# Performance work log

Measured on AMD Instinct MI355X. Metric: run time of the kernel, lower is better.

Reference implementation:

```python
import jax, jax.numpy as jnp
import numpy as np
import math

B, S, D, H = 8, 2048, 256, 8

def setup_inputs() -> dict:
    key = jax.random.key(0)
    k1, k2, k3 = jax.random.split(key, 3)
    e = jax.random.normal(k1, (B, S, D), dtype=jnp.float32)
    p = jax.random.normal(k2, (B, S + 1, D), dtype=jnp.float32)
    n_layer = 12
    W_o = jax.random.normal(k3, (D, D * H), dtype=jnp.float32) * (0.02 / math.sqrt(2 * n_layer))
    return {"e": e, "p": p, "W_o": W_o}

def reference(e, p, W_o):
    # e: [B,S,D], p: [B,S+1,D], W_o: [D, H*D] (nn.Linear weight)
    Bx, Sx, Dx = e.shape
    Hh = W_o.shape[1] // Dx
    # Original builds head-replicated Q=p, K=p[:-1], V=e; all heads compute
    # identical attention, so compute it once and tile for the W_o mix.
    q = p[:, 1:, :]   # rows 1..S of Q survive the [:, :, 1:, :] slice
    k = p[:, :-1, :]  # [B,S,D]
    scores = jnp.einsum('bqd,bkd->bqk', q, k) / math.sqrt(Dx)  # [B,S,S]
    scores = jnp.clip(scores, -10.0, 10.0)  # clamp happens BEFORE masking
    # Mask: tril(diag=-1) rows 1..S-1 plus an all-ones last row == standard
    # causal mask (col <= row) after the row slice.
    causal = jnp.tril(jnp.ones((Sx, Sx), dtype=bool))
    scores = jnp.where(causal[None, :, :], scores, -jnp.inf)
    attn = jax.nn.softmax(scores, axis=-1)
    y = jnp.einsum('bqk,bkd->bqd', attn, e)  # [B,S,D]
    # W_N diagonal matmul == per-row scale by 1/(i+1)
    row_scale = 1.0 / (jnp.arange(Sx, dtype=y.dtype) + 1.0)
    y = y * row_scale[None, :, None]
    y_cat = jnp.tile(y, (1, 1, Hh))  # heads are identical -> [B,S,H*D]
    out = y_cat @ W_o.T  # Linear(H*D -> D), no bias
    return out
```

## Files before the change

### kernel.cpp

```cpp
#include <hip/hip_runtime.h>


typedef __attribute__((ext_vector_type(8))) short short8;
typedef __attribute__((ext_vector_type(4))) float f32x4;

__device__ __forceinline__ unsigned short f2b(float x) {
  unsigned u = __builtin_bit_cast(unsigned, x);
  u = (u + 0x7fffu + ((u >> 16) & 1u)) >> 16;
  return (unsigned short)u;
}

__global__ void cvt_p_kernel(const float* __restrict__ src, unsigned short* __restrict__ dst) {
  size_t t = (size_t)blockIdx.x * 256 + threadIdx.x;
  const float4* s = (const float4*)(src + t * 8);
  float4 a = s[0], b = s[1];
  short8 o;
  o[0] = (short)f2b(a.x); o[1] = (short)f2b(a.y); o[2] = (short)f2b(a.z); o[3] = (short)f2b(a.w);
  o[4] = (short)f2b(b.x); o[5] = (short)f2b(b.y); o[6] = (short)f2b(b.z); o[7] = (short)f2b(b.w);
  *(short8*)(dst + t * 8) = o;
}

__global__ void perm_e_kernel(const float* __restrict__ e, unsigned short* __restrict__ dst) {
  size_t t = (size_t)blockIdx.x * 256 + threadIdx.x;
  int lane = (int)(t & 63);
  int d0 = (int)((t >> 6) & 15);
  int kt = (int)((t >> 10) & 63);
  int b = (int)(t >> 16);
  int g = lane >> 4, l = lane & 15;
  const float* s = e + ((size_t)b * 2048 + kt * 32 + g * 8) * 256 + d0 * 16 + l;
  short8 o;
#pragma unroll
  for (int i = 0; i < 8; ++i) o[i] = (short)f2b(s[(size_t)i * 256]);
  *(short8*)(dst + t * 8) = o;
}

__global__ void perm_k_kernel(const float* __restrict__ p, unsigned short* __restrict__ dst) {
  size_t t = (size_t)blockIdx.x * 256 + threadIdx.x;
  int lane = (int)(t & 63);
  int idx = (int)((t >> 6) & 15);
  int kt = (int)((t >> 10) & 63);
  int b = (int)(t >> 16);
  int kc = idx >> 1, n0 = idx & 1;
  int g = lane >> 4, l = lane & 15;
  const float* s = p + ((size_t)b * 2049 + kt * 32 + n0 * 16 + l) * 256 + kc * 32 + g * 8;
  float4 a = *(const float4*)s;
  float4 c = *(const float4*)(s + 4);
  short8 o;
  o[0] = (short)f2b(a.x); o[1] = (short)f2b(a.y); o[2] = (short)f2b(a.z); o[3] = (short)f2b(a.w);
  o[4] = (short)f2b(c.x); o[5] = (short)f2b(c.y); o[6] = (short)f2b(c.z); o[7] = (short)f2b(c.w);
  *(short8*)(dst + t * 8) = o;
}

__global__ void fold_w_kernel(const float* __restrict__ w, unsigned short* __restrict__ dst) {
  int d = blockIdx.x;
  int c = threadIdx.x;
  const float* row = w + (size_t)d * 2048 + c;
  float s = 0.f;
#pragma unroll
  for (int h = 0; h < 8; ++h) s += row[h * 256];
  dst[d * 256 + c] = f2b(s);
}

#define SMEM_BYTES 25088

__global__ __launch_bounds__(256, 2) void attn_main_kernel(const unsigned short* __restrict__ pbf,
                                                           const unsigned short* __restrict__ kperm,
                                                           const unsigned short* __restrict__ eperm,
                                                           const unsigned short* __restrict__ wsum,
                                                           float* __restrict__ out) {
  __shared__ char smem[SMEM_BYTES];
  const int b = blockIdx.x & 7;
  const int j0 = blockIdx.x >> 3;
  const int t16 = (j0 < 64) ? j0 : 191 - j0;
  const int qbase = t16 * 16;
  const int nkt = (t16 >> 1) + 1;
  const int wave = threadIdx.x >> 6;
  const int lane = threadIdx.x & 63;
  const int g = lane >> 4;
  const int l = lane & 15;
  const f32x4 zero = {0.f, 0.f, 0.f, 0.f};

  short8 qf[8];
  {
    const unsigned short* qrow = pbf + ((size_t)b * 2049 + qbase + l + 1) * 256;
#pragma unroll
    for (int kc = 0; kc < 8; ++kc) qf[kc] = *(const short8*)(qrow + kc * 32 + g * 8);
  }

  f32x4 yacc[16];
#pragma unroll
  for (int i = 0; i < 16; ++i) yacc[i] = zero;
  float dsum[4] = {0.f, 0.f, 0.f, 0.f};

  unsigned short* pp = (unsigned short*)(smem + 16384 + wave * 1280);
  const unsigned short* kpool = kperm + (size_t)b * 64 * 8192 + (size_t)lane * 8;
  const unsigned short* epool = eperm + (size_t)b * 64 * 8192 + (size_t)lane * 8;

  short8 kf[16], ef[16];
  if (wave < nkt) {
    const unsigned short* kb = kpool + (size_t)wave * 8192;
    const unsigned short* eb = epool + (size_t)wave * 8192;
#pragma unroll
    for (int i = 0; i < 16; ++i) kf[i] = *(const short8*)(kb + i * 512);
#pragma unroll
    for (int i = 0; i < 16; ++i) ef[i] = *(const short8*)(eb + i * 512);
  }

  for (int kt = wave; kt < nkt; kt += 4) {
    const int ktn = kt + 4;
    f32x4 sacc0 = zero, sacc1 = zero;
#pragma unroll
    for (int kc = 0; kc < 8; ++kc) {
      sacc0 = __builtin_amdgcn_mfma_f32_16x16x32_bf16(qf[kc], kf[kc * 2 + 0], sacc0, 0, 0, 0);
      sacc1 = __builtin_amdgcn_mfma_f32_16x16x32_bf16(qf[kc], kf[kc * 2 + 1], sacc1, 0, 0, 0);
    }
    if (ktn < nkt) {
      const unsigned short* kb = kpool + (size_t)ktn * 8192;
#pragma unroll
      for (int i = 0; i < 16; ++i) kf[i] = *(const short8*)(kb + i * 512);
    }
#pragma unroll
    for (int n0 = 0; n0 < 2; ++n0) {
      const int kg = kt * 32 + n0 * 16 + l;
      const f32x4 sv = n0 ? sacc1 : sacc0;
#pragma unroll
      for (int jj = 0; jj < 4; ++jj) {
        float s = sv[jj] * 0.0625f;
        s = fminf(fmaxf(s, -10.f), 10.f);
        const int qg = qbase + g * 4 + jj;
        float w = (kg <= qg) ? __expf(s) : 0.f;
        dsum[jj] += w;
        pp[(g * 4 + jj) * 40 + n0 * 16 + l] = f2b(w);
      }
    }
    short8 af = *(const short8*)((const unsigned short*)pp + l * 40 + g * 8);
#pragma unroll
    for (int d0 = 0; d0 < 16; ++d0)
      yacc[d0] = __builtin_amdgcn_mfma_f32_16x16x32_bf16(af, ef[d0], yacc[d0], 0, 0, 0);
    if (ktn < nkt) {
      const unsigned short* eb = epool + (size_t)ktn * 8192;
#pragma unroll
      for (int i = 0; i < 16; ++i) ef[i] = *(const short8*)(eb + i * 512);
    }
  }

#pragma unroll
  for (int jj = 0; jj < 4; ++jj) {
    float v = dsum[jj];
    v += __shfl_xor(v, 1);
    v += __shfl_xor(v, 2);
    v += __shfl_xor(v, 4);
    v += __shfl_xor(v, 8);
    dsum[jj] = v;
  }
  float* dbuf = (float*)(smem + 24832);
  if (wave != 0 && l == 0) {
#pragma unroll
    for (int jj = 0; jj < 4; ++jj) dbuf[(wave - 1) * 16 + g * 4 + jj] = dsum[jj];
  }

  f32x4* bufv = (f32x4*)smem;
  __syncthreads();
  if (wave == 1) {
#pragma unroll
    for (int d0 = 0; d0 < 16; ++d0) bufv[d0 * 64 + lane] = yacc[d0];
  }
  __syncthreads();
  if (wave == 0) {
#pragma unroll
    for (int d0 = 0; d0 < 16; ++d0) yacc[d0] += bufv[d0 * 64 + lane];
  }
  __syncthreads();
  if (wave == 2) {
#pragma unroll
    for (int d0 = 0; d0 < 16; ++d0) bufv[d0 * 64 + lane] = yacc[d0];
  }
  __syncthreads();
  if (wave == 0) {
#pragma unroll
    for (int d0 = 0; d0 < 16; ++d0) yacc[d0] += bufv[d0 * 64 + lane];
  }
  __syncthreads();
  if (wave == 3) {
#pragma unroll
    for (int d0 = 0; d0 < 16; ++d0) bufv[d0 * 64 + lane] = yacc[d0];
  }
  __syncthreads();
  unsigned short* py = (unsigned short*)(smem + 16384);
  if (wave == 0) {
    float inv[4];
#pragma unroll
    for (int jj = 0; jj < 4; ++jj) {
      float dtot = dsum[jj] + dbuf[g * 4 + jj] + dbuf[16 + g * 4 + jj] + dbuf[32 + g * 4 + jj];
      const int qg = qbase + g * 4 + jj;
      inv[jj] = 1.f / (dtot * (float)(qg + 1));
    }
#pragma unroll
    for (int d0 = 0; d0 < 16; ++d0) {
      f32x4 yt = yacc[d0] + bufv[d0 * 64 + lane];
#pragma unroll
      for (int jj = 0; jj < 4; ++jj)
        py[(g * 4 + jj) * 264 + d0 * 16 + l] = f2b(yt[jj] * inv[jj]);
    }
  }
  __syncthreads();

  {
    f32x4 oacc[4];
#pragma unroll
    for (int i = 0; i < 4; ++i) oacc[i] = zero;
#pragma unroll
    for (int kc = 0; kc < 8; ++kc) {
      short8 a2 = *(const short8*)(py + l * 264 + kc * 32 + g * 8);
#pragma unroll
      for (int dd = 0; dd < 4; ++dd) {
        short8 wf =
            *(const short8*)(wsum + (size_t)((wave * 4 + dd) * 16 + l) * 256 + kc * 32 + g * 8);
        oacc[dd] = __builtin_amdgcn_mfma_f32_16x16x32_bf16(a2, wf, oacc[dd], 0, 0, 0);
      }
    }
#pragma unroll
    for (int dd = 0; dd < 4; ++dd) {
#pragma unroll
      for (int jj = 0; jj < 4; ++jj) {
        const int qg = qbase + g * 4 + jj;
        const int d = (wave * 4 + dd) * 16 + l;
        out[((size_t)b * 2048 + qg) * 256 + d] = oacc[dd][jj];
      }
    }
  }
}

extern "C" void kernel_launch(void* const* d_in, const int* in_sizes, int n_in, void* d_out,
                              int out_size, void* d_ws, size_t ws_size, hipStream_t stream) {
  (void)in_sizes; (void)n_in; (void)out_size; (void)ws_size;
  const float* e = (const float*)d_in[0];
  const float* p = (const float*)d_in[1];
  const float* Wo = (const float*)d_in[2];
  float* out = (float*)d_out;

  unsigned short* pbf = (unsigned short*)d_ws;
  unsigned short* eperm = (unsigned short*)((char*)d_ws + 8392704);
  unsigned short* kperm = (unsigned short*)((char*)d_ws + 16781312);
  unsigned short* wsum = (unsigned short*)((char*)d_ws + 25169920);

  hipLaunchKernelGGL(cvt_p_kernel, dim3(2049), dim3(256), 0, stream, p, pbf);
  hipLaunchKernelGGL(perm_e_kernel, dim3(2048), dim3(256), 0, stream, e, eperm);
  hipLaunchKernelGGL(perm_k_kernel, dim3(2048), dim3(256), 0, stream, p, kperm);
  hipLaunchKernelGGL(fold_w_kernel, dim3(256), dim3(256), 0, stream, Wo, wsum);
  hipLaunchKernelGGL(attn_main_kernel, dim3(1024), dim3(256), 0, stream, pbf, kperm, eperm, wsum,
                     out);
}
```

Before: 149.6 us.

## Stage K/V tiles in LDS with double buffering, 32-row query blocks

The attention kernel now gives each block 32 query rows, split across two query-halves of two waves each. K and V tiles are streamed into double-buffered shared memory with global_load_lds, replacing per-wave register prefetch of whole tiles. Each wave covers one 16-column half of the scores and half of the output dimensions, so waves share the staged tiles and the four-way cross-wave reduction of the y accumulators goes away. The cost is more shared memory (about 67KB per block), which may cap occupancy, a barrier every K tile, and half as many blocks in the grid.

```diff
diff --git a/kernel.cpp b/kernel.cpp
--- a/kernel.cpp
+++ b/kernel.cpp
@@ -9,6 +9,10 @@
   u = (u + 0x7fffu + ((u >> 16) & 1u)) >> 16;
   return (unsigned short)u;
 }
+
+#define GLOAD_LDS16(gp, lp)                                                                        \
+  __builtin_amdgcn_global_load_lds((const __attribute__((address_space(1))) unsigned int*)(gp),    \
+                                   (__attribute__((address_space(3))) unsigned int*)(lp), 16, 0, 0)
 
 __global__ void cvt_p_kernel(const float* __restrict__ src, unsigned short* __restrict__ dst) {
   size_t t = (size_t)blockIdx.x * 256 + threadIdx.x;
@@ -61,7 +65,22 @@
   dst[d * 256 + c] = f2b(s);
 }
 
-#define SMEM_BYTES 25088
+#define SMEM_BYTES 68352
+
+__device__ __forceinline__ void stage_tile(char* smem, int s, int b, int kt, int tid,
+                                           const unsigned short* kperm,
+                                           const unsigned short* eperm) {
+  const size_t cb = (size_t)(b * 64 + kt) * 8192;
+  char* kd = smem + s * 32768;
+  const char* ks = (const char*)(kperm + cb);
+  const char* es = (const char*)(eperm + cb);
+  const int wv64 = tid & ~63;
+#pragma unroll
+  for (int j = 0; j < 4; ++j) {
+    GLOAD_LDS16(ks + (j * 256 + tid) * 16, kd + (j * 256 + wv64) * 16);
+    GLOAD_LDS16(es + (j * 256 + tid) * 16, kd + 16384 + (j * 256 + wv64) * 16);
+  }
+}
 
 __global__ __launch_bounds__(256, 2) void attn_main_kernel(const unsigned short* __restrict__ pbf,
                                                            const unsigned short* __restrict__ kperm,
@@ -70,78 +89,71 @@
                                                            float* __restrict__ out) {
   __shared__ char smem[SMEM_BYTES];
   const int b = blockIdx.x & 7;
-  const int j0 = blockIdx.x >> 3;
-  const int t16 = (j0 < 64) ? j0 : 191 - j0;
-  const int qbase = t16 * 16;
-  const int nkt = (t16 >> 1) + 1;
-  const int wave = threadIdx.x >> 6;
-  const int lane = threadIdx.x & 63;
+  const int pr = blockIdx.x >> 3;
+  const int t32 = (pr < 32) ? pr : 95 - pr;
+  const int qbase = t32 * 32;
+  const int nkt = t32 + 1;
+  const int tid = threadIdx.x;
+  const int wave = tid >> 6;
+  const int lane = tid & 63;
+  const int qh = wave >> 1;
+  const int z = wave & 1;
   const int g = lane >> 4;
   const int l = lane & 15;
   const f32x4 zero = {0.f, 0.f, 0.f, 0.f};
 
   short8 qf[8];
   {
-    const unsigned short* qrow = pbf + ((size_t)b * 2049 + qbase + l + 1) * 256;
+    const unsigned short* qrow = pbf + ((size_t)b * 2049 + qbase + qh * 16 + l + 1) * 256;
 #pragma unroll
     for (int kc = 0; kc < 8; ++kc) qf[kc] = *(const short8*)(qrow + kc * 32 + g * 8);
   }
 
-  f32x4 yacc[16];
-#pragma unroll
-  for (int i = 0; i < 16; ++i) yacc[i] = zero;
+  f32x4 yacc[8];
+#pragma unroll
+  for (int i = 0; i < 8; ++i) yacc[i] = zero;
   float dsum[4] = {0.f, 0.f, 0.f, 0.f};
 
-  unsigned short* pp = (unsigned short*)(smem + 16384 + wave * 1280);
-  const unsigned short* kpool = kperm + (size_t)b * 64 * 8192 + (size_t)lane * 8;
-  const unsigned short* epool = eperm + (size_t)b * 64 * 8192 + (size_t)lane * 8;
-
-  short8 kf[16], ef[16];
-  if (wave < nkt) {
-    const unsigned short* kb = kpool + (size_t)wave * 8192;
-    const unsigned short* eb = epool + (size_t)wave * 8192;
-#pragma unroll
-    for (int i = 0; i < 16; ++i) kf[i] = *(const short8*)(kb + i * 512);
-#pragma unroll
-    for (int i = 0; i < 16; ++i) ef[i] = *(const short8*)(eb + i * 512);
-  }
-
-  for (int kt = wave; kt < nkt; kt += 4) {
-    const int ktn = kt + 4;
-    f32x4 sacc0 = zero, sacc1 = zero;
+  unsigned short* pp = (unsigned short*)(smem + 65536 + qh * 1280);
+  const int qrow0 = qbase + qh * 16 + g * 4;
+
+  stage_tile(smem, 0, b, 0, tid, kperm, eperm);
+  asm volatile("s_waitcnt vmcnt(0)" ::: "memory");
+  __builtin_amdgcn_s_barrier();
+
+  for (int kt = 0; kt < nkt; ++kt) {
+    const int cur = kt & 1;
+    if (kt + 1 < nkt) stage_tile(smem, cur ^ 1, b, kt + 1, tid, kperm, eperm);
+
+    const char* kb = smem + cur * 32768;
+    f32x4 sacc = zero;
 #pragma unroll
     for (int kc = 0; kc < 8; ++kc) {
-      sacc0 = __builtin_amdgcn_mfma_f32_16x16x32_bf16(qf[kc], kf[kc * 2 + 0], sacc0, 0, 0, 0);
-      sacc1 = __builtin_amdgcn_mfma_f32_16x16x32_bf16(qf[kc], kf[kc * 2 + 1], sacc1, 0, 0, 0);
-    }
-    if (ktn < nkt) {
-      const unsigned short* kb = kpool + (size_t)ktn * 8192;
-#pragma unroll
-      for (int i = 0; i < 16; ++i) kf[i] = *(const short8*)(kb + i * 512);
-    }
-#pragma unroll
-    for (int n0 = 0; n0 < 2; ++n0) {
-      const int kg = kt * 32 + n0 * 16 + l;
-      const f32x4 sv = n0 ? sacc1 : sacc0;
-#pragma unroll
-      for (int jj = 0; jj < 4; ++jj) {
-        float s = sv[jj] * 0.0625f;
-        s = fminf(fmaxf(s, -10.f), 10.f);
-        const int qg = qbase + g * 4 + jj;
-        float w = (kg <= qg) ? __expf(s) : 0.f;
-        dsum[jj] += w;
-        pp[(g * 4 + jj) * 40 + n0 * 16 + l] = f2b(w);
-      }
-    }
-    short8 af = *(const short8*)((const unsigned short*)pp + l * 40 + g * 8);
-#pragma unroll
-    for (int d0 = 0; d0 < 16; ++d0)
-      yacc[d0] = __builtin_amdgcn_mfma_f32_16x16x32_bf16(af, ef[d0], yacc[d0], 0, 0, 0);
-    if (ktn < nkt) {
-      const unsigned short* eb = epool + (size_t)ktn * 8192;
-#pragma unroll
-      for (int i = 0; i < 16; ++i) ef[i] = *(const short8*)(eb + i * 512);
-    }
+      short8 kf = *(const short8*)(kb + (kc * 2 + z) * 1024 + lane * 16);
+      sacc = __builtin_amdgcn_mfma_f32_16x16x32_bf16(qf[kc], kf, sacc, 0, 0, 0);
+    }
+    const int kg = kt * 32 + z * 16 + l;
+#pragma unroll
+    for (int jj = 0; jj < 4; ++jj) {
+      float s = sacc[jj] * 0.0625f;
+      s = fminf(fmaxf(s, -10.f), 10.f);
+      float w = (kg <= qrow0 + jj) ? __expf(s) : 0.f;
+      dsum[jj] += w;
+      pp[(g * 4 + jj) * 40 + z * 16 + l] = f2b(w);
+    }
+    asm volatile("s_waitcnt lgkmcnt(0)" ::: "memory");
+    __builtin_amdgcn_s_barrier();
+    __builtin_amdgcn_sched_barrier(0);
+
+    short8 af = *(const short8*)(pp + l * 40 + g * 8);
+    const char* eb = smem + cur * 32768 + 16384;
+#pragma unroll
+    for (int dd = 0; dd < 8; ++dd) {
+      short8 ef = *(const short8*)(eb + (z * 8 + dd) * 1024 + lane * 16);
+      yacc[dd] = __builtin_amdgcn_mfma_f32_16x16x32_bf16(af, ef, yacc[dd], 0, 0, 0);
+    }
+    asm volatile("s_waitcnt vmcnt(0) lgkmcnt(0)" ::: "memory");
+    __builtin_amdgcn_s_barrier();
   }
 
 #pragma unroll
@@ -153,79 +165,50 @@
     v += __shfl_xor(v, 8);
     dsum[jj] = v;
   }
-  float* dbuf = (float*)(smem + 24832);
-  if (wave != 0 && l == 0) {
-#pragma unroll
-    for (int jj = 0; jj < 4; ++jj) dbuf[(wave - 1) * 16 + g * 4 + jj] = dsum[jj];
-  }
-
-  f32x4* bufv = (f32x4*)smem;
+  float* dx = (float*)(smem + 68096);
+  if (l == 0) {
+#pragma unroll
+    for (int jj = 0; jj < 4; ++jj) dx[(qh * 2 + z) * 16 + g * 4 + jj] = dsum[jj];
+  }
   __syncthreads();
-  if (wave == 1) {
-#pragma unroll
-    for (int d0 = 0; d0 < 16; ++d0) bufv[d0 * 64 + lane] = yacc[d0];
+
+  unsigned short* py = (unsigned short*)smem;
+  {
+    float inv[4];
+#pragma unroll
+    for (int jj = 0; jj < 4; ++jj) {
+      float dtot = dx[(qh * 2) * 16 + g * 4 + jj] + dx[(qh * 2 + 1) * 16 + g * 4 + jj];
+      inv[jj] = 1.f / (dtot * (float)(qrow0 + jj + 1));
+    }
+#pragma unroll
+    for (int dd = 0; dd < 8; ++dd) {
+#pragma unroll
+      for (int jj = 0; jj < 4; ++jj)
+        py[(qh * 16 + g * 4 + jj) * 260 + (z * 8 + dd) * 16 + l] = f2b(yacc[dd][jj] * inv[jj]);
+    }
   }
   __syncthreads();
-  if (wave == 0) {
-#pragma unroll
-    for (int d0 = 0; d0 < 16; ++d0) yacc[d0] += bufv[d0 * 64 + lane];
-  }
-  __syncthreads();
-  if (wave == 2) {
-#pragma unroll
-    for (int d0 = 0; d0 < 16; ++d0) bufv[d0 * 64 + lane] = yacc[d0];
-  }
-  __syncthreads();
-  if (wave == 0) {
-#pragma unroll
-    for (int d0 = 0; d0 < 16; ++d0) yacc[d0] += bufv[d0 * 64 + lane];
-  }
-  __syncthreads();
-  if (wave == 3) {
-#pragma unroll
-    for (int d0 = 0; d0 < 16; ++d0) bufv[d0 * 64 + lane] = yacc[d0];
-  }
-  __syncthreads();
-  unsigned short* py = (unsigned short*)(smem + 16384);
-  if (wave == 0) {
-    float inv[4];
-#pragma unroll
-    for (int jj = 0; jj < 4; ++jj) {
-      float dtot = dsum[jj] + dbuf[g * 4 + jj] + dbuf[16 + g * 4 + jj] + dbuf[32 + g * 4 + jj];
-      const int qg = qbase + g * 4 + jj;
-      inv[jj] = 1.f / (dtot * (float)(qg + 1));
-    }
-#pragma unroll
-    for (int d0 = 0; d0 < 16; ++d0) {
-      f32x4 yt = yacc[d0] + bufv[d0 * 64 + lane];
-#pragma unroll
-      for (int jj = 0; jj < 4; ++jj)
-        py[(g * 4 + jj) * 264 + d0 * 16 + l] = f2b(yt[jj] * inv[jj]);
-    }
-  }
-  __syncthreads();
 
   {
-    f32x4 oacc[4];
-#pragma unroll
-    for (int i = 0; i < 4; ++i) oacc[i] = zero;
+    f32x4 oacc[8];
+#pragma unroll
+    for (int i = 0; i < 8; ++i) oacc[i] = zero;
 #pragma unroll
     for (int kc = 0; kc < 8; ++kc) {
-      short8 a2 = *(const short8*)(py + l * 264 + kc * 32 + g * 8);
-#pragma unroll
-      for (int dd = 0; dd < 4; ++dd) {
+      short8 a2 = *(const short8*)(py + (qh * 16 + l) * 260 + kc * 32 + g * 8);
+#pragma unroll
+      for (int dd = 0; dd < 8; ++dd) {
         short8 wf =
-            *(const short8*)(wsum + (size_t)((wave * 4 + dd) * 16 + l) * 256 + kc * 32 + g * 8);
+            *(const short8*)(wsum + (size_t)((z * 8 + dd) * 16 + l) * 256 + kc * 32 + g * 8);
         oacc[dd] = __builtin_amdgcn_mfma_f32_16x16x32_bf16(a2, wf, oacc[dd], 0, 0, 0);
       }
     }
 #pragma unroll
-    for (int dd = 0; dd < 4; ++dd) {
+    for (int dd = 0; dd < 8; ++dd) {
 #pragma unroll
       for (int jj = 0; jj < 4; ++jj) {
-        const int qg = qbase + g * 4 + jj;
-        const int d = (wave * 4 + dd) * 16 + l;
-        out[((size_t)b * 2048 + qg) * 256 + d] = oacc[dd][jj];
+        const int d = (z * 8 + dd) * 16 + l;
+        out[((size_t)b * 2048 + qbase + qh * 16 + g * 4 + jj) * 256 + d] = oacc[dd][jj];
       }
     }
   }
@@ -248,6 +231,6 @@
   hipLaunchKernelGGL(perm_e_kernel, dim3(2048), dim3(256), 0, stream, e, eperm);
   hipLaunchKernelGGL(perm_k_kernel, dim3(2048), dim3(256), 0, stream, p, kperm);
   hipLaunchKernelGGL(fold_w_kernel, dim3(256), dim3(256), 0, stream, Wo, wsum);
-  hipLaunchKernelGGL(attn_main_kernel, dim3(1024), dim3(256), 0, stream, pbf, kperm, eperm, wsum,
+  hipLaunchKernelGGL(attn_main_kernel, dim3(512), dim3(256), 0, stream, pbf, kperm, eperm, wsum,
                      out);
 }
```

Result: no change. 152.1 us (+1.7%).
